# Kernel tuning notes

Hardware: AMD Instinct MI355X
Metric: run time of the kernel (lower is better)

The kernel has to match this reference:

```python
import jax, jax.numpy as jnp
import numpy as np

B, Q, P = 8, 300, 5
RS, QS, CS, NC = 256, 768, 768, 396
HW = [64, 32, 16, 8]
POOL = [32, 16, 8, 4]
THR = 0.2


def _ln(x, g, b, eps=1e-5):
    m = x.mean(-1, keepdims=True)
    v = ((x - m) ** 2).mean(-1, keepdims=True)
    return (x - m) / jnp.sqrt(v + eps) * g + b


def _avgpool(x, oh, ow):
    # exact adaptive avg pool (output divides input)
    b, c, h, w = x.shape
    return x.reshape(b, c, oh, h // oh, ow, w // ow).mean((3, 5))


def setup_inputs() -> dict:
    key = jax.random.key(0)
    ks = jax.random.split(key, 40)
    inp = {}
    inp['pred_logits'] = jax.random.normal(ks[0], (B, Q, P), dtype=jnp.float32)
    inp['pred_boxes'] = jax.random.uniform(ks[1], (B, Q, 4), dtype=jnp.float32)
    inp['hs'] = jax.random.normal(ks[2], (B, Q, RS), dtype=jnp.float32)
    for s in range(4):
        inp[f'feat{s}'] = jax.random.normal(ks[3 + s], (B, 256, HW[s], HW[s]), dtype=jnp.float32)
        inp[f'pos{s}'] = jax.random.normal(ks[7 + s], (B, 256, HW[s], HW[s]), dtype=jnp.float32)
        inp[f'mask{s}'] = jax.random.bernoulli(ks[11 + s], 0.15, (B, HW[s], HW[s]))
        inp[f'convW{s}'] = jax.random.normal(ks[15 + s], (CS, 256), dtype=jnp.float32) * 0.02
        inp[f'convb{s}'] = jnp.zeros((CS,), jnp.float32)
        inp[f'lng{s}'] = jnp.ones((CS,), jnp.float32)
        inp[f'lnb{s}'] = jnp.zeros((CS,), jnp.float32)
    inp['learnable_query'] = jax.random.normal(ks[19], (P + 1, QS), dtype=jnp.float32)
    inp['Wq'] = jax.random.normal(ks[20], (RS, QS), dtype=jnp.float32) * 0.02
    inp['bq'] = jnp.zeros((QS,), jnp.float32)
    inp['qng'] = jnp.ones((QS,), jnp.float32)
    inp['qnb'] = jnp.zeros((QS,), jnp.float32)
    inp['W1'] = jax.random.normal(ks[21], (QS, QS), dtype=jnp.float32) * 0.02
    inp['b1'] = jnp.zeros((QS,), jnp.float32)
    inp['W2'] = jax.random.normal(ks[22], (QS, NC), dtype=jnp.float32) * 0.02
    inp['b2'] = jnp.zeros((NC,), jnp.float32)
    return inp


def _forward(pred_logits, pred_boxes, hs,
             feats, poss, masks, convWs, convbs, lngs, lnbs,
             learnable_query, Wq, bq, qng, qnb, W1, b1, W2, b2):
    del pred_boxes  # selected in the original but never used
    b = hs.shape[0]
    prob = jax.nn.sigmoid(pred_logits)                       # (B,Q,P)
    # per-prompt membership: logit_i > thr (implies max > thr)
    m = (prob > THR).astype(hs.dtype)                        # (B,Q,P)
    cnt = m.sum(1)                                           # (B,P)
    ssum = jnp.einsum('bqp,bqd->bpd', m, hs)                 # segment-sum over queries
    pooled = jnp.where(cnt[..., None] > 0,
                       ssum / jnp.maximum(cnt, 1.0)[..., None], 0.0)  # (B,P,RS)
    proj = pooled @ Wq + bq                                  # (B,P,QS)
    any_sel = jnp.any(prob.max(-1) > THR, axis=1)            # (B,)
    # if no query passed the global gate, prompt_hs is zeros WITHOUT projection
    prompt_hs = jnp.where(any_sel[:, None, None], proj, 0.0)
    prompt_query = learnable_query[1:] + prompt_hs           # (B,P,QS)
    cls_query = jnp.broadcast_to(learnable_query[0][None, None, :], (b, 1, QS))
    query_tokens = jnp.concatenate([cls_query, prompt_query], axis=1)
    query_tokens = _ln(query_tokens, qng, qnb)               # (B,P+1,QS)

    tokens = []
    for s in range(4):
        mask_f = masks[s][:, None, :, :].astype(feats[s].dtype)   # (B,1,H,W)
        x = (feats[s] + poss[s]) * (1.0 - mask_f)                 # masked_fill
        ctx = jnp.einsum('bchw,oc->bohw', x, convWs[s]) + convbs[s][None, :, None, None]
        p = _avgpool(ctx, POOL[s], POOL[s])
        mp = jnp.clip(_avgpool(1.0 - mask_f, POOL[s], POOL[s]), 1e-6, None)
        p = p / mp
        t = p.reshape(b, CS, -1).transpose(0, 2, 1)               # (B,T_s,CS)
        tokens.append(_ln(t, lngs[s], lnbs[s]))
    ctx_all = jnp.concatenate(tokens, axis=1)                     # (B,1360,CS)

    # encoder stand-in: fuse context into query tokens additively
    last = query_tokens + ctx_all.mean(1)[:, None, :]
    cls_logit = last[:, 0]
    prompt_logit = last[:, 1:].mean(1)
    h = jax.nn.relu((cls_logit + prompt_logit) @ W1 + b1)
    return h @ W2 + b2                                            # (B,NC)


def reference(pred_logits, pred_boxes, hs,
              feat0, pos0, mask0, convW0, convb0, lng0, lnb0,
              feat1, pos1, mask1, convW1, convb1, lng1, lnb1,
              feat2, pos2, mask2, convW2, convb2, lng2, lnb2,
              feat3, pos3, mask3, convW3, convb3, lng3, lnb3,
              learnable_query, Wq, bq, qng, qnb, W1, b1, W2, b2):
    return _forward(pred_logits, pred_boxes, hs,
                    [feat0, feat1, feat2, feat3],
                    [pos0, pos1, pos2, pos3],
                    [mask0, mask1, mask2, mask3],
                    [convW0, convW1, convW2, convW3],
                    [convb0, convb1, convb2, convb3],
                    [lng0, lng1, lng2, lng3],
                    [lnb0, lnb1, lnb2, lnb3],
                    learnable_query, Wq, bq, qng, qnb, W1, b1, W2, b2)
```

## Files before the change

kernel.cpp:

```cpp
#include <hip/hip_runtime.h>
#include <hip/hip_bf16.h>

#define Bn 8
#define Qn 300
#define Pn 5
#define RSn 256
#define QSn 768
#define NCn 396
#define MTOT 10880
#define THRL -1.3862943611198906f

typedef __attribute__((ext_vector_type(8))) short short8;
typedef __attribute__((ext_vector_type(4))) float float4v;

__device__ inline float wred(float v){
  #pragma unroll
  for (int off = 32; off; off >>= 1) v += __shfl_xor(v, off);
  return v;
}

__device__ __forceinline__ unsigned short f2bf(float f){
  union { float f; unsigned int u; } c; c.f = f;
  return (unsigned short)((c.u + 0x7FFF + ((c.u >> 16) & 1)) >> 16);
}

__device__ __forceinline__ void gld_lds16(const short* g, short* l){
  __builtin_amdgcn_global_load_lds(
      (const __attribute__((address_space(1))) void*)g,
      (__attribute__((address_space(3))) void*)l, 16, 0, 0);
}

__global__ void k_front(const float* cw0, const float* cw1, const float* cw2, const float* cw3,
                        short* Wswz, const int* __restrict__ m0, int* det,
                        const float* __restrict__ pl, const float* __restrict__ hs,
                        float* pooled, int* flags, float* ctxsum){
  int bx = blockIdx.x;
  int t = threadIdx.x;
  if (bx < 768){
    int s = bx / 192;
    int linear = (bx % 192)*256 + t;
    int q = linear & 63, n = linear >> 6;
    const float* src = (s==0)?cw0:(s==1)?cw1:(s==2)?cw2:cw3;
    float4 f = *(const float4*)(src + (size_t)n*256 + q*4);
    int kc = q >> 3, lk = (q >> 1) & 3, e0 = (q & 1)*4;
    short* dst = Wswz + ((size_t)(s*8 + kc))*24576 + lk*6144 + n*8 + e0;
    short4 sv;
    sv.x = (short)f2bf(f.x); sv.y = (short)f2bf(f.y);
    sv.z = (short)f2bf(f.z); sv.w = (short)f2bf(f.w);
    *(short4*)dst = sv;
    return;
  }
  if (bx == 768){
    __shared__ int r0[4], r1[4];
    const int* mm = m0 + t*32;
    int d0 = 0, d1 = 0;
    #pragma unroll 8
    for (int i = 0; i < 32; ++i){
      int v = mm[i];
      d0 |= (v != 0 && v != 1);
      d1 |= (v != 0 && v != 0x3F800000);
    }
    unsigned long long bal0 = __ballot(d0), bal1 = __ballot(d1);
    int wid = t >> 6;
    if ((t & 63) == 0){ r0[wid] = (bal0 != 0ull); r1[wid] = (bal1 != 0ull); }
    __syncthreads();
    if (t == 0){
      det[0] = r0[0] | r0[1] | r0[2] | r0[3];
      det[1] = r1[0] | r1[1] | r1[2] | r1[3];
    }
    return;
  }
  if (bx >= 809){
    int idx = ((bx - 809)*256 + t)*4;
    *(float4*)(ctxsum + idx) = (float4){0.f,0.f,0.f,0.f};
    return;
  }
  __shared__ float msk[Qn];
  int bb = (bx - 769) / Pn, p = (bx - 769) % Pn;
  for (int q = t; q < Qn; q += 256)
    msk[q] = (pl[(bb*Qn + q)*Pn + p] > THRL) ? 1.f : 0.f;
  __syncthreads();
  const float* hb = hs + (size_t)bb*Qn*RSn + t;
  float ssum = 0.f, cnt = 0.f;
  for (int q = 0; q < Qn; ++q){
    float m = msk[q];
    cnt += m;
    ssum = fmaf(m, hb[(size_t)q*RSn], ssum);
  }
  pooled[(bb*Pn + p)*RSn + t] = (cnt > 0.f) ? ssum / cnt : 0.f;
  if (t == 0) flags[bb*Pn + p] = (cnt > 0.f) ? 1 : 0;
}

__global__ void k_mid(const float* f0, const float* p0, const void* m0,
                      const float* f1, const float* p1, const void* m1,
                      const float* f2, const float* p2, const void* m2,
                      const float* f3, const float* p3, const void* m3,
                      const int* __restrict__ det, unsigned short* ATb, float* invmp,
                      const float* __restrict__ lq, const float* __restrict__ Wq,
                      const float* __restrict__ bq, const float* __restrict__ qng,
                      const float* __restrict__ qnb, const float* __restrict__ pooled,
                      const int* __restrict__ flags, float* qt){
  __shared__ float pq[256];
  __shared__ float s1[4], s2[4];
  int bx = blockIdx.x;
  int t = threadIdx.x;
  if (bx >= 48){
    int p = bx - 48;
    int s = p >> 9, b = (p >> 6) & 7, c0 = (p & 63) << 2;
    const float* F; const float* Pp; const void* M; int H, SB;
    if (s == 0){ F=f0; Pp=p0; M=m0; H=64; SB=0;     }
    else if (s == 1){ F=f1; Pp=p1; M=m1; H=32; SB=8192;  }
    else if (s == 2){ F=f2; Pp=p2; M=m2; H=16; SB=10240; }
    else            { F=f3; Pp=p3; M=m3; H=8;  SB=10752; }
    int OW = H >> 1, T = OW * OW;
    int OW2 = OW >> 1, T2 = T >> 1;
    int HH = H*H;
    int mode = (det[0] == 0) ? 0 : ((det[1] == 0) ? 2 : 1);
    size_t plane = (size_t)(b*256 + c0)*HH;
    const float* Fb = F + plane;
    const float* Pb = Pp + plane;
    int mbase = b*HH;
    for (int tk = t; tk < T2; tk += 256){
      int ph = tk / OW2, pw = tk - ph*OW2;
      int i00 = (ph*2)*H + pw*4;
      float w[8];
      if (mode == 0){
        int4 ma = *(const int4*)((const int*)M + mbase + i00);
        int4 mb = *(const int4*)((const int*)M + mbase + i00 + H);
        w[0]=ma.x?0.f:1.f; w[1]=ma.y?0.f:1.f; w[2]=ma.z?0.f:1.f; w[3]=ma.w?0.f:1.f;
        w[4]=mb.x?0.f:1.f; w[5]=mb.y?0.f:1.f; w[6]=mb.z?0.f:1.f; w[7]=mb.w?0.f:1.f;
      } else if (mode == 1){
        const unsigned char* Mb = (const unsigned char*)M + mbase;
        uchar4 ma = *(const uchar4*)(Mb + i00);
        uchar4 mb = *(const uchar4*)(Mb + i00 + H);
        w[0]=ma.x?0.f:1.f; w[1]=ma.y?0.f:1.f; w[2]=ma.z?0.f:1.f; w[3]=ma.w?0.f:1.f;
        w[4]=mb.x?0.f:1.f; w[5]=mb.y?0.f:1.f; w[6]=mb.z?0.f:1.f; w[7]=mb.w?0.f:1.f;
      } else {
        float4 ma = *(const float4*)((const float*)M + mbase + i00);
        float4 mb = *(const float4*)((const float*)M + mbase + i00 + H);
        w[0]=1.f-ma.x; w[1]=1.f-ma.y; w[2]=1.f-ma.z; w[3]=1.f-ma.w;
        w[4]=1.f-mb.x; w[5]=1.f-mb.y; w[6]=1.f-mb.z; w[7]=1.f-mb.w;
      }
      float ms0 = w[0]+w[1]+w[4]+w[5];
      float ms1 = w[2]+w[3]+w[6]+w[7];
      float im0 = 1.f / fmaxf(ms0*0.25f, 1e-6f);
      float im1 = 1.f / fmaxf(ms1*0.25f, 1e-6f);
      float sc0 = 0.25f*im0, sc1 = 0.25f*im1;
      int mIdx = SB + b*T + tk*2;
      #pragma unroll
      for (int cc = 0; cc < 4; ++cc){
        const float* Fc = Fb + cc*HH;
        const float* Pc = Pb + cc*HH;
        float4 fa  = *(const float4*)(Fc + i00);
        float4 fb2 = *(const float4*)(Fc + i00 + H);
        float4 pa  = *(const float4*)(Pc + i00);
        float4 pb2 = *(const float4*)(Pc + i00 + H);
        float x0 = (fa.x+pa.x)*w[0] + (fa.y+pa.y)*w[1] + (fb2.x+pb2.x)*w[4] + (fb2.y+pb2.y)*w[5];
        float x1 = (fa.z+pa.z)*w[2] + (fa.w+pa.w)*w[3] + (fb2.z+pb2.z)*w[6] + (fb2.w+pb2.w)*w[7];
        *(unsigned int*)(ATb + (size_t)(c0+cc)*MTOT + mIdx) =
            (unsigned int)f2bf(x0*sc0) | ((unsigned int)f2bf(x1*sc1) << 16);
      }
      if (c0 == 0){ invmp[mIdx] = im0; invmp[mIdx+1] = im1; }
    }
    return;
  }
  int b = bx / 6, j = bx % 6;
  float v0 = lq[j*QSn + t], v1 = lq[j*QSn + t + 256], v2 = lq[j*QSn + t + 512];
  int any = flags[b*Pn] | flags[b*Pn+1] | flags[b*Pn+2] | flags[b*Pn+3] | flags[b*Pn+4];
  if (j > 0 && any){
    pq[t] = pooled[(b*Pn + (j-1))*RSn + t];
    __syncthreads();
    float a0 = 0.f, a1 = 0.f, a2 = 0.f;
    #pragma unroll 8
    for (int c = 0; c < RSn; ++c){
      float pv = pq[c];
      a0 = fmaf(pv, Wq[c*QSn + t      ], a0);
      a1 = fmaf(pv, Wq[c*QSn + t + 256], a1);
      a2 = fmaf(pv, Wq[c*QSn + t + 512], a2);
    }
    v0 += a0 + bq[t]; v1 += a1 + bq[t+256]; v2 += a2 + bq[t+512];
  }
  float sm = v0 + v1 + v2, sq = v0*v0 + v1*v1 + v2*v2;
  sm = wred(sm); sq = wred(sq);
  int wid = t >> 6, lane = t & 63;
  if (lane == 0){ s1[wid] = sm; s2[wid] = sq; }
  __syncthreads();
  float S  = s1[0] + s1[1] + s1[2] + s1[3];
  float SQ = s2[0] + s2[1] + s2[2] + s2[3];
  float mu = S * (1.f/QSn), var = SQ * (1.f/QSn) - mu*mu;
  float rs = rsqrtf(var + 1e-5f);
  float* o = qt + (b*6 + j)*QSn;
  o[t      ] = (v0 - mu)*rs*qng[t      ] + qnb[t      ];
  o[t + 256] = (v1 - mu)*rs*qng[t + 256] + qnb[t + 256];
  o[t + 512] = (v2 - mu)*rs*qng[t + 512] + qnb[t + 512];
}

__global__ __launch_bounds__(256, 2) void k_gemm_ln(
    const unsigned short* __restrict__ ATb, const short* __restrict__ Wswz,
    const float* __restrict__ invmp,
    const float* cb0, const float* cb1, const float* cb2, const float* cb3,
    const float* lg0, const float* lb0, const float* lg1, const float* lb1,
    const float* lg2, const float* lb2, const float* lg3, const float* lb3,
    float* __restrict__ ctxsum){
  __shared__ short Bsh[24576];
  __shared__ float lsum[4][32], lsq[4][32];
  int m0 = blockIdx.x * 32;
  int s;
  if (m0 < 8192) s = 0;
  else if (m0 < 10240) s = 1;
  else if (m0 < 10752) s = 2;
  else s = 3;
  int b0, b1;
  if (s == 0){ b0 = m0 >> 10; b1 = b0; }
  else if (s == 1){ b0 = (m0 - 8192) >> 8; b1 = b0; }
  else if (s == 2){ b0 = (m0 - 10240) >> 6; b1 = b0; }
  else { b0 = (m0 - 10752) >> 4; b1 = b0 + 1; }
  const float *CB, *LG, *LB;
  if (s==0){ CB=cb0; LG=lg0; LB=lb0; }
  else if (s==1){ CB=cb1; LG=lg1; LB=lb1; }
  else if (s==2){ CB=cb2; LG=lg2; LB=lb2; }
  else { CB=cb3; LG=lg3; LB=lb3; }

  int t = threadIdx.x;
  int wid = t >> 6, l = t & 63;
  int lm = l & 15, lk = l >> 4;
  int nfb = wid * 12;

  {
    const unsigned short* src = ATb + (size_t)t*MTOT + m0;
    short8 a0 = *(const short8*)(src);
    short8 a1 = *(const short8*)(src + 8);
    short8 a2 = *(const short8*)(src + 16);
    short8 a3 = *(const short8*)(src + 24);
    #pragma unroll
    for (int e = 0; e < 8; ++e){
      Bsh[e*264 + t]      = a0[e];
      Bsh[(e+8)*264 + t]  = a1[e];
      Bsh[(e+16)*264 + t] = a2[e];
      Bsh[(e+24)*264 + t] = a3[e];
    }
  }
  __syncthreads();
  short8 aReg[2][8];
  #pragma unroll
  for (int mt = 0; mt < 2; ++mt)
    #pragma unroll
    for (int kc = 0; kc < 8; ++kc)
      aReg[mt][kc] = *(const short8*)(Bsh + (mt*16 + lm)*264 + kc*32 + lk*8);
  __syncthreads();

  float4v acc[2][12];
  #pragma unroll
  for (int mt = 0; mt < 2; ++mt)
    #pragma unroll
    for (int nf = 0; nf < 12; ++nf) acc[mt][nf] = (float4v){0.f,0.f,0.f,0.f};

  #pragma unroll
  for (int kc = 0; kc < 8; ++kc){
    const short* slice = Wswz + ((size_t)(s*8 + kc))*24576;
    #pragma unroll
    for (int j = 0; j < 12; ++j){
      int chunk = wid*12 + j;
      gld_lds16(slice + chunk*512 + l*8, Bsh + chunk*512);
    }
    __syncthreads();
    const short* bb = Bsh + lk*6144 + lm*8;
    #pragma unroll
    for (int nf = 0; nf < 12; ++nf){
      short8 bf = *(const short8*)(bb + (size_t)(nfb+nf)*128);
      acc[0][nf] = __builtin_amdgcn_mfma_f32_16x16x32_bf16(aReg[0][kc], bf, acc[0][nf], 0, 0, 0);
      acc[1][nf] = __builtin_amdgcn_mfma_f32_16x16x32_bf16(aReg[1][kc], bf, acc[1][nf], 0, 0, 0);
    }
    __syncthreads();
  }

  float im[2][4];
  #pragma unroll
  for (int mt = 0; mt < 2; ++mt)
    #pragma unroll
    for (int r = 0; r < 4; ++r) im[mt][r] = invmp[m0 + mt*16 + lk*4 + r];

  float sum[2][4] = {{0,0,0,0},{0,0,0,0}}, sq[2][4] = {{0,0,0,0},{0,0,0,0}};
  #pragma unroll
  for (int nf = 0; nf < 12; ++nf){
    float cbv = CB[(nfb+nf)*16 + lm];
    #pragma unroll
    for (int mt = 0; mt < 2; ++mt)
      #pragma unroll
      for (int r = 0; r < 4; ++r){
        float p = acc[mt][nf][r] + cbv*im[mt][r];
        acc[mt][nf][r] = p;
        sum[mt][r] += p;
        sq[mt][r] = fmaf(p, p, sq[mt][r]);
      }
  }
  #pragma unroll
  for (int mt = 0; mt < 2; ++mt)
    #pragma unroll
    for (int r = 0; r < 4; ++r){
      #pragma unroll
      for (int off = 1; off < 16; off <<= 1){
        sum[mt][r] += __shfl_xor(sum[mt][r], off);
        sq[mt][r]  += __shfl_xor(sq[mt][r],  off);
      }
    }
  if (lm == 0){
    #pragma unroll
    for (int mt = 0; mt < 2; ++mt)
      #pragma unroll
      for (int r = 0; r < 4; ++r){
        lsum[wid][mt*16 + lk*4 + r] = sum[mt][r];
        lsq[wid][mt*16 + lk*4 + r]  = sq[mt][r];
      }
  }
  __syncthreads();
  float mu[2][4], rs[2][4];
  #pragma unroll
  for (int mt = 0; mt < 2; ++mt)
    #pragma unroll
    for (int r = 0; r < 4; ++r){
      int row = mt*16 + lk*4 + r;
      float S  = lsum[0][row] + lsum[1][row] + lsum[2][row] + lsum[3][row];
      float SQ = lsq[0][row]  + lsq[1][row]  + lsq[2][row]  + lsq[3][row];
      mu[mt][r] = S * (1.f/768.f);
      float var = SQ * (1.f/768.f) - mu[mt][r]*mu[mt][r];
      rs[mt][r] = rsqrtf(var + 1e-5f);
    }
  #pragma unroll
  for (int nf = 0; nf < 12; ++nf){
    int n = (nfb+nf)*16 + lm;
    float g = LG[n], bb2 = LB[n];
    float tv0 = 0.f, tv1 = 0.f;
    #pragma unroll
    for (int r = 0; r < 4; ++r){
      tv0 += (acc[0][nf][r] - mu[0][r]) * rs[0][r];
      tv1 += (acc[1][nf][r] - mu[1][r]) * rs[1][r];
    }
    tv0 = tv0*g + 4.f*bb2;
    tv1 = tv1*g + 4.f*bb2;
    tv0 += __shfl_xor(tv0, 16); tv0 += __shfl_xor(tv0, 32);
    tv1 += __shfl_xor(tv1, 16); tv1 += __shfl_xor(tv1, 32);
    if (lk == 0){
      atomicAdd(&ctxsum[b0*768 + n], tv0);
      atomicAdd(&ctxsum[b1*768 + n], tv1);
    }
  }
}

__global__ void k_hpre(const float* __restrict__ qt, const float* __restrict__ ctxsum,
                       const float* __restrict__ W1, const float* __restrict__ b1,
                       float* __restrict__ hpre){
  __shared__ float vsh[Bn][768];
  __shared__ float part[4][Bn][32];
  int n0 = blockIdx.x * 32;
  int t = threadIdx.x;
  for (int i = t; i < Bn*768; i += 256){
    int b = i / 768, c = i - b*768;
    const float* q = qt + (size_t)b*6*768;
    float pm = q[768+c] + q[2*768+c] + q[3*768+c] + q[4*768+c] + q[5*768+c];
    vsh[b][c] = q[c] + 0.2f*pm + ctxsum[b*768 + c]*(1.f/680.f);
  }
  __syncthreads();
  int ow = t & 31, half = (t >> 5) & 1, kq = t >> 6;
  int o = n0 + ow, c0 = kq*192;
  float acc[4] = {0,0,0,0};
  const float* w = W1 + (size_t)c0*768 + o;
  #pragma unroll 4
  for (int cl = 0; cl < 192; ++cl){
    float wv = w[(size_t)cl*768];
    #pragma unroll
    for (int bi = 0; bi < 4; ++bi)
      acc[bi] = fmaf(vsh[half*4+bi][c0+cl], wv, acc[bi]);
  }
  #pragma unroll
  for (int bi = 0; bi < 4; ++bi) part[kq][half*4+bi][ow] = acc[bi];
  __syncthreads();
  int b = t >> 5, oo = t & 31;
  float v = part[0][b][oo] + part[1][b][oo] + part[2][b][oo] + part[3][b][oo] + b1[n0+oo];
  hpre[b*768 + n0 + oo] = v;
}

__global__ void k_out(const float* __restrict__ hpre, const float* __restrict__ W2,
                      const float* __restrict__ b2, float* __restrict__ out){
  __shared__ float hsh[Bn][768];
  __shared__ float part[4][Bn][32];
  int n0 = blockIdx.x * 32;
  int t = threadIdx.x;
  for (int i = t; i < Bn*768; i += 256)
    hsh[0][i] = fmaxf(hpre[i], 0.f);
  __syncthreads();
  int ow = t & 31, half = (t >> 5) & 1, kq = t >> 6;
  int o = n0 + ow, c0 = kq*192;
  float acc[4] = {0,0,0,0};
  if (o < NCn){
    const float* w = W2 + (size_t)c0*NCn + o;
    #pragma unroll 4
    for (int cl = 0; cl < 192; ++cl){
      float wv = w[(size_t)cl*NCn];
      #pragma unroll
      for (int bi = 0; bi < 4; ++bi)
        acc[bi] = fmaf(hsh[half*4+bi][c0+cl], wv, acc[bi]);
    }
  }
  #pragma unroll
  for (int bi = 0; bi < 4; ++bi) part[kq][half*4+bi][ow] = acc[bi];
  __syncthreads();
  int b = t >> 5, oo = t & 31;
  int oc = n0 + oo;
  if (oc < NCn){
    float v = part[0][b][oo] + part[1][b][oo] + part[2][b][oo] + part[3][b][oo] + b2[oc];
    out[b*NCn + oc] = v;
  }
}

extern "C" void kernel_launch(void* const* d_in, const int* in_sizes, int n_in,
                              void* d_out, int out_size, void* d_ws, size_t ws_size,
                              hipStream_t stream){
  const float* pl = (const float*)d_in[0];
  const float* hs = (const float*)d_in[2];
  const float* feat[4]; const float* pos[4]; const void* mask[4];
  const float* cw[4]; const float* cb[4]; const float* lg[4]; const float* lb[4];
  for (int s = 0; s < 4; ++s){
    int base = 3 + 7*s;
    feat[s] = (const float*)d_in[base];
    pos[s]  = (const float*)d_in[base+1];
    mask[s] = d_in[base+2];
    cw[s]   = (const float*)d_in[base+3];
    cb[s]   = (const float*)d_in[base+4];
    lg[s]   = (const float*)d_in[base+5];
    lb[s]   = (const float*)d_in[base+6];
  }
  const float* lq  = (const float*)d_in[31];
  const float* Wq  = (const float*)d_in[32];
  const float* bq  = (const float*)d_in[33];
  const float* qng = (const float*)d_in[34];
  const float* qnb = (const float*)d_in[35];
  const float* W1  = (const float*)d_in[36];
  const float* b1  = (const float*)d_in[37];
  const float* W2  = (const float*)d_in[38];
  const float* b2  = (const float*)d_in[39];
  float* out = (float*)d_out;

  unsigned short* ATb = (unsigned short*)d_ws;
  short* Wswz   = (short*)(ATb + (size_t)256*MTOT);
  float* invmp  = (float*)(Wswz + (size_t)4*8*4*768*8);
  float* pooled = invmp + MTOT;
  float* qt     = pooled + 40*RSn;
  float* ctxsum = qt + Bn*6*QSn;
  int*   det    = (int*)(ctxsum + Bn*QSn);
  int*   flags  = det + 4;
  float* hpre   = (float*)(flags + 40);

  k_front<<<815, 256, 0, stream>>>(cw[0], cw[1], cw[2], cw[3], Wswz,
                                   (const int*)mask[0], det, pl, hs, pooled, flags, ctxsum);
  k_mid<<<2096, 256, 0, stream>>>(feat[0], pos[0], mask[0],
                                  feat[1], pos[1], mask[1],
                                  feat[2], pos[2], mask[2],
                                  feat[3], pos[3], mask[3],
                                  det, ATb, invmp,
                                  lq, Wq, bq, qng, qnb, pooled, flags, qt);
  k_gemm_ln<<<340, 256, 0, stream>>>(ATb, Wswz, invmp,
                                     cb[0], cb[1], cb[2], cb[3],
                                     lg[0], lb[0], lg[1], lb[1],
                                     lg[2], lb[2], lg[3], lb[3], ctxsum);
  k_hpre<<<24, 256, 0, stream>>>(qt, ctxsum, W1, b1, hpre);
  k_out<<<13, 256, 0, stream>>>(hpre, W2, b2, out);
}
```

Measured before the change: 292.4 us.

## Split-K atomics for tail GEMVs and re-partition pooling work per scale

The two small tail GEMV kernels are split along K into 4 chunks (96 and 52 blocks instead of 24 and 13), with partial sums combined through atomicAdd into buffers zeroed earlier in k_front. k_mid's pooling path now uses a fixed per-scale thread mapping that issues all feature and position loads up front instead of a strided per-block loop. The masked-mean loop in k_front uses four independent accumulators, and launch bounds are added. The intent is to expose more parallelism in latency-bound tail kernels and memory-level parallelism in pooling. The cost is atomic contention and a non-deterministic summation order.

Result: faster. 285.6 us (-2.3%).

```diff
diff --git a/kernel.cpp b/kernel.cpp
--- a/kernel.cpp
+++ b/kernel.cpp
@@ -30,10 +30,32 @@
       (__attribute__((address_space(3))) void*)l, 16, 0, 0);
 }
 
-__global__ void k_front(const float* cw0, const float* cw1, const float* cw2, const float* cw3,
-                        short* Wswz, const int* __restrict__ m0, int* det,
-                        const float* __restrict__ pl, const float* __restrict__ hs,
-                        float* pooled, int* flags, float* ctxsum){
+__device__ __forceinline__ void mask_w(const void* M, int mbase, int mode, int i00, int H,
+                                       float* w){
+  if (mode == 0){
+    int4 ma = *(const int4*)((const int*)M + mbase + i00);
+    int4 mb = *(const int4*)((const int*)M + mbase + i00 + H);
+    w[0]=ma.x?0.f:1.f; w[1]=ma.y?0.f:1.f; w[2]=ma.z?0.f:1.f; w[3]=ma.w?0.f:1.f;
+    w[4]=mb.x?0.f:1.f; w[5]=mb.y?0.f:1.f; w[6]=mb.z?0.f:1.f; w[7]=mb.w?0.f:1.f;
+  } else if (mode == 1){
+    const unsigned char* Mb = (const unsigned char*)M + mbase;
+    uchar4 ma = *(const uchar4*)(Mb + i00);
+    uchar4 mb = *(const uchar4*)(Mb + i00 + H);
+    w[0]=ma.x?0.f:1.f; w[1]=ma.y?0.f:1.f; w[2]=ma.z?0.f:1.f; w[3]=ma.w?0.f:1.f;
+    w[4]=mb.x?0.f:1.f; w[5]=mb.y?0.f:1.f; w[6]=mb.z?0.f:1.f; w[7]=mb.w?0.f:1.f;
+  } else {
+    float4 ma = *(const float4*)((const float*)M + mbase + i00);
+    float4 mb = *(const float4*)((const float*)M + mbase + i00 + H);
+    w[0]=1.f-ma.x; w[1]=1.f-ma.y; w[2]=1.f-ma.z; w[3]=1.f-ma.w;
+    w[4]=1.f-mb.x; w[5]=1.f-mb.y; w[6]=1.f-mb.z; w[7]=1.f-mb.w;
+  }
+}
+
+__global__ __launch_bounds__(256, 4) void k_front(
+    const float* cw0, const float* cw1, const float* cw2, const float* cw3,
+    short* Wswz, const int* __restrict__ m0, int* det,
+    const float* __restrict__ pl, const float* __restrict__ hs,
+    float* pooled, int* flags, float* ctxsum, float* outz){
   int bx = blockIdx.x;
   int t = threadIdx.x;
   if (bx < 768){
@@ -70,6 +92,11 @@
     }
     return;
   }
+  if (bx >= 821){
+    int idx = ((bx - 821)*256 + t)*4;
+    if (idx < Bn*NCn) *(float4*)(outz + idx) = (float4){0.f,0.f,0.f,0.f};
+    return;
+  }
   if (bx >= 809){
     int idx = ((bx - 809)*256 + t)*4;
     *(float4*)(ctxsum + idx) = (float4){0.f,0.f,0.f,0.f};
@@ -81,87 +108,158 @@
     msk[q] = (pl[(bb*Qn + q)*Pn + p] > THRL) ? 1.f : 0.f;
   __syncthreads();
   const float* hb = hs + (size_t)bb*Qn*RSn + t;
-  float ssum = 0.f, cnt = 0.f;
-  for (int q = 0; q < Qn; ++q){
-    float m = msk[q];
-    cnt += m;
-    ssum = fmaf(m, hb[(size_t)q*RSn], ssum);
-  }
+  float s0 = 0.f, s1 = 0.f, s2 = 0.f, s3 = 0.f, cnt = 0.f;
+  for (int q = 0; q < Qn; q += 4){
+    float m0v = msk[q], m1 = msk[q+1], m2 = msk[q+2], m3 = msk[q+3];
+    cnt += m0v + m1 + m2 + m3;
+    s0 = fmaf(m0v, hb[(size_t)(q  )*RSn], s0);
+    s1 = fmaf(m1,  hb[(size_t)(q+1)*RSn], s1);
+    s2 = fmaf(m2,  hb[(size_t)(q+2)*RSn], s2);
+    s3 = fmaf(m3,  hb[(size_t)(q+3)*RSn], s3);
+  }
+  float ssum = (s0 + s1) + (s2 + s3);
   pooled[(bb*Pn + p)*RSn + t] = (cnt > 0.f) ? ssum / cnt : 0.f;
   if (t == 0) flags[bb*Pn + p] = (cnt > 0.f) ? 1 : 0;
 }
 
-__global__ void k_mid(const float* f0, const float* p0, const void* m0,
-                      const float* f1, const float* p1, const void* m1,
-                      const float* f2, const float* p2, const void* m2,
-                      const float* f3, const float* p3, const void* m3,
-                      const int* __restrict__ det, unsigned short* ATb, float* invmp,
-                      const float* __restrict__ lq, const float* __restrict__ Wq,
-                      const float* __restrict__ bq, const float* __restrict__ qng,
-                      const float* __restrict__ qnb, const float* __restrict__ pooled,
-                      const int* __restrict__ flags, float* qt){
+__global__ __launch_bounds__(256, 4) void k_mid(
+    const float* f0, const float* p0, const void* m0,
+    const float* f1, const float* p1, const void* m1,
+    const float* f2, const float* p2, const void* m2,
+    const float* f3, const float* p3, const void* m3,
+    const int* __restrict__ det, unsigned short* ATb, float* invmp,
+    const float* __restrict__ lq, const float* __restrict__ Wq,
+    const float* __restrict__ bq, const float* __restrict__ qng,
+    const float* __restrict__ qnb, const float* __restrict__ pooled,
+    const int* __restrict__ flags, float* qt){
   __shared__ float pq[256];
-  __shared__ float s1[4], s2[4];
+  __shared__ float s1s[4], s2s[4];
   int bx = blockIdx.x;
   int t = threadIdx.x;
   if (bx >= 48){
     int p = bx - 48;
-    int s = p >> 9, b = (p >> 6) & 7, c0 = (p & 63) << 2;
-    const float* F; const float* Pp; const void* M; int H, SB;
-    if (s == 0){ F=f0; Pp=p0; M=m0; H=64; SB=0;     }
-    else if (s == 1){ F=f1; Pp=p1; M=m1; H=32; SB=8192;  }
-    else if (s == 2){ F=f2; Pp=p2; M=m2; H=16; SB=10240; }
-    else            { F=f3; Pp=p3; M=m3; H=8;  SB=10752; }
-    int OW = H >> 1, T = OW * OW;
-    int OW2 = OW >> 1, T2 = T >> 1;
-    int HH = H*H;
     int mode = (det[0] == 0) ? 0 : ((det[1] == 0) ? 2 : 1);
-    size_t plane = (size_t)(b*256 + c0)*HH;
-    const float* Fb = F + plane;
-    const float* Pb = Pp + plane;
-    int mbase = b*HH;
-    for (int tk = t; tk < T2; tk += 256){
-      int ph = tk / OW2, pw = tk - ph*OW2;
-      int i00 = (ph*2)*H + pw*4;
+    if (p < 1024){
+      int b = p >> 7, r = p & 127;
+      int c0 = (r >> 1)*4, half = r & 1;
+      const int H = 64, HH = 4096;
+      int tk = half*256 + t;
+      int ph = tk >> 4, pw = tk & 15;
+      int i00 = ph*128 + pw*4;
+      int mbase = b*HH;
       float w[8];
-      if (mode == 0){
-        int4 ma = *(const int4*)((const int*)M + mbase + i00);
-        int4 mb = *(const int4*)((const int*)M + mbase + i00 + H);
-        w[0]=ma.x?0.f:1.f; w[1]=ma.y?0.f:1.f; w[2]=ma.z?0.f:1.f; w[3]=ma.w?0.f:1.f;
-        w[4]=mb.x?0.f:1.f; w[5]=mb.y?0.f:1.f; w[6]=mb.z?0.f:1.f; w[7]=mb.w?0.f:1.f;
-      } else if (mode == 1){
-        const unsigned char* Mb = (const unsigned char*)M + mbase;
-        uchar4 ma = *(const uchar4*)(Mb + i00);
-        uchar4 mb = *(const uchar4*)(Mb + i00 + H);
-        w[0]=ma.x?0.f:1.f; w[1]=ma.y?0.f:1.f; w[2]=ma.z?0.f:1.f; w[3]=ma.w?0.f:1.f;
-        w[4]=mb.x?0.f:1.f; w[5]=mb.y?0.f:1.f; w[6]=mb.z?0.f:1.f; w[7]=mb.w?0.f:1.f;
-      } else {
-        float4 ma = *(const float4*)((const float*)M + mbase + i00);
-        float4 mb = *(const float4*)((const float*)M + mbase + i00 + H);
-        w[0]=1.f-ma.x; w[1]=1.f-ma.y; w[2]=1.f-ma.z; w[3]=1.f-ma.w;
-        w[4]=1.f-mb.x; w[5]=1.f-mb.y; w[6]=1.f-mb.z; w[7]=1.f-mb.w;
-      }
+      mask_w(m0, mbase, mode, i00, H, w);
+      size_t plane = (size_t)(b*256 + c0)*HH + i00;
+      const float* Fb = f0 + plane;
+      const float* Pb = p0 + plane;
+      float4 FA0 = *(const float4*)(Fb);
+      float4 FB0 = *(const float4*)(Fb + H);
+      float4 PA0 = *(const float4*)(Pb);
+      float4 PB0 = *(const float4*)(Pb + H);
+      float4 FA1 = *(const float4*)(Fb + HH);
+      float4 FB1 = *(const float4*)(Fb + HH + H);
+      float4 PA1 = *(const float4*)(Pb + HH);
+      float4 PB1 = *(const float4*)(Pb + HH + H);
+      float4 FA2 = *(const float4*)(Fb + 2*HH);
+      float4 FB2 = *(const float4*)(Fb + 2*HH + H);
+      float4 PA2 = *(const float4*)(Pb + 2*HH);
+      float4 PB2 = *(const float4*)(Pb + 2*HH + H);
+      float4 FA3 = *(const float4*)(Fb + 3*HH);
+      float4 FB3 = *(const float4*)(Fb + 3*HH + H);
+      float4 PA3 = *(const float4*)(Pb + 3*HH);
+      float4 PB3 = *(const float4*)(Pb + 3*HH + H);
+      float ms0 = w[0]+w[1]+w[4]+w[5];
+      float ms1 = w[2]+w[3]+w[6]+w[7];
+      float im0 = 1.f / fmaxf(ms0*0.25f, 1e-6f);
+      float im1 = 1.f / fmaxf(ms1*0.25f, 1e-6f);
+      float sc0 = 0.25f*im0, sc1 = 0.25f*im1;
+      int mIdx = b*1024 + tk*2;
+      #define DO_CH(cc, FA, FB, PA, PB) { \
+        float x0 = (FA.x+PA.x)*w[0] + (FA.y+PA.y)*w[1] + (FB.x+PB.x)*w[4] + (FB.y+PB.y)*w[5]; \
+        float x1 = (FA.z+PA.z)*w[2] + (FA.w+PA.w)*w[3] + (FB.z+PB.z)*w[6] + (FB.w+PB.w)*w[7]; \
+        *(unsigned int*)(ATb + (size_t)(c0+cc)*MTOT + mIdx) = \
+            (unsigned int)f2bf(x0*sc0) | ((unsigned int)f2bf(x1*sc1) << 16); }
+      DO_CH(0, FA0, FB0, PA0, PB0)
+      DO_CH(1, FA1, FB1, PA1, PB1)
+      DO_CH(2, FA2, FB2, PA2, PB2)
+      DO_CH(3, FA3, FB3, PA3, PB3)
+      #undef DO_CH
+      if (c0 == 0){ invmp[mIdx] = im0; invmp[mIdx+1] = im1; }
+      return;
+    }
+    const float* F; const float* Pp; const void* M; int H, SB, T;
+    int b, ch, tk; bool wr;
+    if (p < 1536){
+      int idx = p - 1024; b = idx >> 6;
+      int c0 = (idx & 63)*4;
+      F=f1; Pp=p1; M=m1; H=32; SB=8192; T=256;
+      int ci = t >> 7; tk = t & 127;
+      ch = c0 + ci*2; wr = (ch == 0);
+      int ph = tk >> 3, pw = tk & 7;
+      int i00 = ph*64 + pw*4;
+      int HH = H*H, mbase = b*HH;
+      float w[8]; mask_w(M, mbase, mode, i00, H, w);
       float ms0 = w[0]+w[1]+w[4]+w[5];
       float ms1 = w[2]+w[3]+w[6]+w[7];
       float im0 = 1.f / fmaxf(ms0*0.25f, 1e-6f);
       float im1 = 1.f / fmaxf(ms1*0.25f, 1e-6f);
       float sc0 = 0.25f*im0, sc1 = 0.25f*im1;
       int mIdx = SB + b*T + tk*2;
-      #pragma unroll
-      for (int cc = 0; cc < 4; ++cc){
-        const float* Fc = Fb + cc*HH;
-        const float* Pc = Pb + cc*HH;
-        float4 fa  = *(const float4*)(Fc + i00);
-        float4 fb2 = *(const float4*)(Fc + i00 + H);
-        float4 pa  = *(const float4*)(Pc + i00);
-        float4 pb2 = *(const float4*)(Pc + i00 + H);
-        float x0 = (fa.x+pa.x)*w[0] + (fa.y+pa.y)*w[1] + (fb2.x+pb2.x)*w[4] + (fb2.y+pb2.y)*w[5];
-        float x1 = (fa.z+pa.z)*w[2] + (fa.w+pa.w)*w[3] + (fb2.z+pb2.z)*w[6] + (fb2.w+pb2.w)*w[7];
-        *(unsigned int*)(ATb + (size_t)(c0+cc)*MTOT + mIdx) =
+      size_t plane = (size_t)(b*256 + ch)*HH + i00;
+      const float* Fb = F + plane; const float* Pb = Pp + plane;
+      float4 FA0 = *(const float4*)(Fb);
+      float4 FB0 = *(const float4*)(Fb + H);
+      float4 PA0 = *(const float4*)(Pb);
+      float4 PB0 = *(const float4*)(Pb + H);
+      float4 FA1 = *(const float4*)(Fb + HH);
+      float4 FB1 = *(const float4*)(Fb + HH + H);
+      float4 PA1 = *(const float4*)(Pb + HH);
+      float4 PB1 = *(const float4*)(Pb + HH + H);
+      {
+        float x0 = (FA0.x+PA0.x)*w[0] + (FA0.y+PA0.y)*w[1] + (FB0.x+PB0.x)*w[4] + (FB0.y+PB0.y)*w[5];
+        float x1 = (FA0.z+PA0.z)*w[2] + (FA0.w+PA0.w)*w[3] + (FB0.z+PB0.z)*w[6] + (FB0.w+PB0.w)*w[7];
+        *(unsigned int*)(ATb + (size_t)ch*MTOT + mIdx) =
             (unsigned int)f2bf(x0*sc0) | ((unsigned int)f2bf(x1*sc1) << 16);
+        float y0 = (FA1.x+PA1.x)*w[0] + (FA1.y+PA1.y)*w[1] + (FB1.x+PB1.x)*w[4] + (FB1.y+PB1.y)*w[5];
+        float y1 = (FA1.z+PA1.z)*w[2] + (FA1.w+PA1.w)*w[3] + (FB1.z+PB1.z)*w[6] + (FB1.w+PB1.w)*w[7];
+        *(unsigned int*)(ATb + (size_t)(ch+1)*MTOT + mIdx) =
+            (unsigned int)f2bf(y0*sc0) | ((unsigned int)f2bf(y1*sc1) << 16);
       }
-      if (c0 == 0){ invmp[mIdx] = im0; invmp[mIdx+1] = im1; }
-    }
+      if (wr){ invmp[mIdx] = im0; invmp[mIdx+1] = im1; }
+      return;
+    }
+    if (p < 1792){
+      int idx = p - 1536; b = idx >> 5;
+      ch = ((idx & 31)*8) + (t >> 5); tk = t & 31;
+      F=f2; Pp=p2; M=m2; H=16; SB=10240; T=64;
+    } else {
+      int idx = p - 1792; b = idx >> 3;
+      ch = ((idx & 7)*32) + (t >> 3); tk = t & 7;
+      F=f3; Pp=p3; M=m3; H=8; SB=10752; T=16;
+    }
+    wr = (ch == 0);
+    int OW2 = H >> 2;
+    int ph = tk / OW2, pw = tk - ph*OW2;
+    int i00 = ph*2*H + pw*4;
+    int HH = H*H, mbase = b*HH;
+    float w[8]; mask_w(M, mbase, mode, i00, H, w);
+    float ms0 = w[0]+w[1]+w[4]+w[5];
+    float ms1 = w[2]+w[3]+w[6]+w[7];
+    float im0 = 1.f / fmaxf(ms0*0.25f, 1e-6f);
+    float im1 = 1.f / fmaxf(ms1*0.25f, 1e-6f);
+    float sc0 = 0.25f*im0, sc1 = 0.25f*im1;
+    int mIdx = SB + b*T + tk*2;
+    size_t plane = (size_t)(b*256 + ch)*HH + i00;
+    const float* Fb = F + plane; const float* Pb = Pp + plane;
+    float4 FA = *(const float4*)(Fb);
+    float4 FB = *(const float4*)(Fb + H);
+    float4 PA = *(const float4*)(Pb);
+    float4 PB = *(const float4*)(Pb + H);
+    float x0 = (FA.x+PA.x)*w[0] + (FA.y+PA.y)*w[1] + (FB.x+PB.x)*w[4] + (FB.y+PB.y)*w[5];
+    float x1 = (FA.z+PA.z)*w[2] + (FA.w+PA.w)*w[3] + (FB.z+PB.z)*w[6] + (FB.w+PB.w)*w[7];
+    *(unsigned int*)(ATb + (size_t)ch*MTOT + mIdx) =
+        (unsigned int)f2bf(x0*sc0) | ((unsigned int)f2bf(x1*sc1) << 16);
+    if (wr){ invmp[mIdx] = im0; invmp[mIdx+1] = im1; }
     return;
   }
   int b = bx / 6, j = bx % 6;
@@ -183,10 +281,10 @@
   float sm = v0 + v1 + v2, sq = v0*v0 + v1*v1 + v2*v2;
   sm = wred(sm); sq = wred(sq);
   int wid = t >> 6, lane = t & 63;
-  if (lane == 0){ s1[wid] = sm; s2[wid] = sq; }
-  __syncthreads();
-  float S  = s1[0] + s1[1] + s1[2] + s1[3];
-  float SQ = s2[0] + s2[1] + s2[2] + s2[3];
+  if (lane == 0){ s1s[wid] = sm; s2s[wid] = sq; }
+  __syncthreads();
+  float S  = s1s[0] + s1s[1] + s1s[2] + s1s[3];
+  float SQ = s2s[0] + s2s[1] + s2s[2] + s2s[3];
   float mu = S * (1.f/QSn), var = SQ * (1.f/QSn) - mu*mu;
   float rs = rsqrtf(var + 1e-5f);
   float* o = qt + (b*6 + j)*QSn;
@@ -350,67 +448,50 @@
 __global__ void k_hpre(const float* __restrict__ qt, const float* __restrict__ ctxsum,
                        const float* __restrict__ W1, const float* __restrict__ b1,
                        float* __restrict__ hpre){
-  __shared__ float vsh[Bn][768];
-  __shared__ float part[4][Bn][32];
-  int n0 = blockIdx.x * 32;
+  __shared__ float vsh[Bn][192];
+  int nc = blockIdx.x % 24, kc = blockIdx.x / 24;
+  int n0 = nc*32, c0 = kc*192;
   int t = threadIdx.x;
-  for (int i = t; i < Bn*768; i += 256){
-    int b = i / 768, c = i - b*768;
+  for (int i = t; i < Bn*192; i += 256){
+    int b = i / 192, cl = i - b*192;
+    int c = c0 + cl;
     const float* q = qt + (size_t)b*6*768;
     float pm = q[768+c] + q[2*768+c] + q[3*768+c] + q[4*768+c] + q[5*768+c];
-    vsh[b][c] = q[c] + 0.2f*pm + ctxsum[b*768 + c]*(1.f/680.f);
-  }
-  __syncthreads();
-  int ow = t & 31, half = (t >> 5) & 1, kq = t >> 6;
-  int o = n0 + ow, c0 = kq*192;
-  float acc[4] = {0,0,0,0};
+    vsh[b][cl] = q[c] + 0.2f*pm + ctxsum[b*768 + c]*(1.f/680.f);
+  }
+  __syncthreads();
+  int ow = t & 31, bi = t >> 5;
+  int o = n0 + ow;
+  float acc = 0.f;
   const float* w = W1 + (size_t)c0*768 + o;
   #pragma unroll 4
-  for (int cl = 0; cl < 192; ++cl){
-    float wv = w[(size_t)cl*768];
-    #pragma unroll
-    for (int bi = 0; bi < 4; ++bi)
-      acc[bi] = fmaf(vsh[half*4+bi][c0+cl], wv, acc[bi]);
-  }
-  #pragma unroll
-  for (int bi = 0; bi < 4; ++bi) part[kq][half*4+bi][ow] = acc[bi];
-  __syncthreads();
-  int b = t >> 5, oo = t & 31;
-  float v = part[0][b][oo] + part[1][b][oo] + part[2][b][oo] + part[3][b][oo] + b1[n0+oo];
-  hpre[b*768 + n0 + oo] = v;
+  for (int cl = 0; cl < 192; ++cl)
+    acc = fmaf(vsh[bi][cl], w[(size_t)cl*768], acc);
+  if (kc == 0) acc += b1[o];
+  atomicAdd(&hpre[bi*768 + o], acc);
 }
 
 __global__ void k_out(const float* __restrict__ hpre, const float* __restrict__ W2,
                       const float* __restrict__ b2, float* __restrict__ out){
-  __shared__ float hsh[Bn][768];
-  __shared__ float part[4][Bn][32];
-  int n0 = blockIdx.x * 32;
+  __shared__ float hsh[Bn][192];
+  int nc = blockIdx.x % 13, kc = blockIdx.x / 13;
+  int n0 = nc*32, c0 = kc*192;
   int t = threadIdx.x;
-  for (int i = t; i < Bn*768; i += 256)
-    hsh[0][i] = fmaxf(hpre[i], 0.f);
-  __syncthreads();
-  int ow = t & 31, half = (t >> 5) & 1, kq = t >> 6;
-  int o = n0 + ow, c0 = kq*192;
-  float acc[4] = {0,0,0,0};
-  if (o < NCn){
-    const float* w = W2 + (size_t)c0*NCn + o;
-    #pragma unroll 4
-    for (int cl = 0; cl < 192; ++cl){
-      float wv = w[(size_t)cl*NCn];
-      #pragma unroll
-      for (int bi = 0; bi < 4; ++bi)
-        acc[bi] = fmaf(hsh[half*4+bi][c0+cl], wv, acc[bi]);
-    }
-  }
-  #pragma unroll
-  for (int bi = 0; bi < 4; ++bi) part[kq][half*4+bi][ow] = acc[bi];
-  __syncthreads();
-  int b = t >> 5, oo = t & 31;
-  int oc = n0 + oo;
-  if (oc < NCn){
-    float v = part[0][b][oo] + part[1][b][oo] + part[2][b][oo] + part[3][b][oo] + b2[oc];
-    out[b*NCn + oc] = v;
-  }
+  for (int i = t; i < Bn*192; i += 256){
+    int b = i / 192, cl = i - b*192;
+    hsh[b][cl] = fmaxf(hpre[b*768 + c0 + cl], 0.f);
+  }
+  __syncthreads();
+  int ow = t & 31, bi = t >> 5;
+  int o = n0 + ow;
+  if (o >= NCn) return;
+  float acc = 0.f;
+  const float* w = W2 + (size_t)c0*NCn + o;
+  #pragma unroll 4
+  for (int cl = 0; cl < 192; ++cl)
+    acc = fmaf(hsh[bi][cl], w[(size_t)cl*NCn], acc);
+  if (kc == 0) acc += b2[o];
+  atomicAdd(&out[bi*NCn + o], acc);
 }
 
 extern "C" void kernel_launch(void* const* d_in, const int* in_sizes, int n_in,
@@ -447,13 +528,14 @@
   float* pooled = invmp + MTOT;
   float* qt     = pooled + 40*RSn;
   float* ctxsum = qt + Bn*6*QSn;
-  int*   det    = (int*)(ctxsum + Bn*QSn);
+  float* hpre   = ctxsum + Bn*QSn;
+  int*   det    = (int*)(hpre + Bn*QSn);
   int*   flags  = det + 4;
-  float* hpre   = (float*)(flags + 40);
-
-  k_front<<<815, 256, 0, stream>>>(cw[0], cw[1], cw[2], cw[3], Wswz,
-                                   (const int*)mask[0], det, pl, hs, pooled, flags, ctxsum);
-  k_mid<<<2096, 256, 0, stream>>>(feat[0], pos[0], mask[0],
+
+  k_front<<<825, 256, 0, stream>>>(cw[0], cw[1], cw[2], cw[3], Wswz,
+                                   (const int*)mask[0], det, pl, hs, pooled, flags,
+                                   ctxsum, out);
+  k_mid<<<1904, 256, 0, stream>>>(feat[0], pos[0], mask[0],
                                   feat[1], pos[1], mask[1],
                                   feat[2], pos[2], mask[2],
                                   feat[3], pos[3], mask[3],
@@ -463,6 +545,6 @@
                                      cb[0], cb[1], cb[2], cb[3],
                                      lg[0], lb[0], lg[1], lb[1],
                                      lg[2], lb[2], lg[3], lb[3], ctxsum);
-  k_hpre<<<24, 256, 0, stream>>>(qt, ctxsum, W1, b1, hpre);
-  k_out<<<13, 256, 0, stream>>>(hpre, W2, b2, out);
-}
+  k_hpre<<<96, 256, 0, stream>>>(qt, ctxsum, W1, b1, hpre);
+  k_out<<<52, 256, 0, stream>>>(hpre, W2, b2, out);
+}
```
